# Kernel optimization log

Measured on AMD Instinct MI355X. Metric: run time of the kernel, lower is better.

Reference implementation:

```python
import jax, jax.numpy as jnp
import numpy as np

B, K, D, L = 512, 64, 1024, 8
LR, WD, STEPS = 1e-4, 0.01, 20


def setup_inputs() -> dict:
    key = jax.random.key(0)
    k1, k2, k3, k4, k5 = jax.random.split(key, 5)
    demo_embeddings = jax.random.normal(k1, (B, K, D), dtype=jnp.float32)
    demo_labels = jax.random.randint(k2, (B, K), 0, L, dtype=jnp.int32)
    embeddings = jax.random.normal(k3, (B, D), dtype=jnp.float32)
    # per-sample fresh nn.Linear init: U(-1/sqrt(D), 1/sqrt(D))
    bound = 1.0 / np.sqrt(D)
    W0 = jax.random.uniform(k4, (B, L, D), dtype=jnp.float32, minval=-bound, maxval=bound)
    b0 = jax.random.uniform(k5, (B, L), dtype=jnp.float32, minval=-bound, maxval=bound)
    return {"demo_embeddings": demo_embeddings, "embeddings": embeddings,
            "W0": W0, "b0": b0, "demo_labels": demo_labels}


def reference(demo_embeddings, embeddings, W0, b0, demo_labels):
    # one-hot targets for MSE branch: [B, K, L]
    Y = jax.nn.one_hot(demo_labels, L, dtype=jnp.float32)
    scale = 2.0 / (K * L)  # d(mean((out-Y)^2))/d(out) factor

    def sgd_step(carry, _):
        W, b = carry  # W: [B, L, D], b: [B, L]
        out = jnp.einsum('bkd,bld->bkl', demo_embeddings, W) + b[:, None, :]
        diff = out - Y
        gW = scale * jnp.einsum('bkl,bkd->bld', diff, demo_embeddings) + WD * W
        gb = scale * diff.sum(axis=1) + WD * b
        return (W - LR * gW, b - LR * gb), None

    (W, b), _ = jax.lax.scan(sgd_step, (W0, b0), None, length=STEPS)
    # predict each query with its own trained linear model
    logits = jnp.einsum('bd,bld->bl', embeddings, W) + b  # [B, L]
    return logits
```

## Files before the change

kernel.cpp:

```cpp
#include <hip/hip_runtime.h>


#define BB 512
#define KK 64
#define DD 1024
#define LL 8
#define NSTEPS 20

typedef __attribute__((ext_vector_type(8))) short bf16x8;
typedef __attribute__((ext_vector_type(4))) float f32x4;

__device__ __forceinline__ short f2bf(float f) {
    unsigned u = __float_as_uint(f);
    unsigned r = (u + 0x7FFFu + ((u >> 16) & 1u)) >> 16;
    return (short)r;
}

struct Chunk {
    float4 x0, x1, x2, x3;
    float4 p;
};

__global__ __launch_bounds__(256, 2)
void knn_linear_fix_kernel(const float* __restrict__ demo,
                           const float* __restrict__ emb,
                           const float* __restrict__ W0,
                           const float* __restrict__ b0,
                           const int*   __restrict__ labels,
                           float* __restrict__ out)
{
    const int b    = blockIdx.x;
    const int t    = threadIdx.x;
    const int lane = t & 63;
    const int wid  = t >> 6;
    const int lg   = lane >> 4;
    const int lr   = lane & 15;

    const float LR  = 1e-4f;
    const float WD  = 0.01f;
    const float LRS = LR * (2.0f / (float)(KK * LL));
    const float CD  = 1.0f - LR * WD;

    __shared__ short Xs[64 * 72];
    __shared__ short Ps[16 * 72];
    __shared__ short Gs[64 * 72];
    __shared__ short Ss[16 * 72];
    __shared__ float red[256];
    __shared__ float p0_s[16];
    __shared__ float q_s[64];
    __shared__ int   lab_s[64];

    const float* Xg = demo + (size_t)b * (KK * DD);
    const float* Wg = W0   + (size_t)b * (LL * DD);
    const float* eg = emb  + (size_t)b * DD;

    if (t < 64) lab_s[t] = labels[b * KK + t];
    for (int i = t; i < 16 * 72; i += 256) Ss[i] = 0;

    float bc = (lr < 8) ? b0[b * LL + lr] : 0.0f;

    f32x4 accG0 = {0,0,0,0}, accG1 = {0,0,0,0}, accG2 = {0,0,0,0}, accG3 = {0,0,0,0};
    f32x4 accM  = {0,0,0,0}, accPP = {0,0,0,0};

    const int xr = t >> 4;
    const int xc = (t & 15) * 4;

#define LOADX(buf, CH) do {                                                      \
        const int dk = (CH) * 64;                                                \
        (buf).x0 = *(const float4*)(Xg + (size_t)(xr     ) * DD + dk + xc);      \
        (buf).x1 = *(const float4*)(Xg + (size_t)(xr + 16) * DD + dk + xc);      \
        (buf).x2 = *(const float4*)(Xg + (size_t)(xr + 32) * DD + dk + xc);      \
        (buf).x3 = *(const float4*)(Xg + (size_t)(xr + 48) * DD + dk + xc);      \
        if (xr < 8)       (buf).p = *(const float4*)(Wg + (size_t)xr * DD + dk + xc); \
        else if (xr == 8) (buf).p = *(const float4*)(eg + dk + xc);              \
        else              (buf).p = make_float4(0.f, 0.f, 0.f, 0.f);             \
    } while (0)

#define STOREC(buf) do {                                                         \
        short4 h;                                                                \
        h.x = f2bf((buf).x0.x); h.y = f2bf((buf).x0.y);                          \
        h.z = f2bf((buf).x0.z); h.w = f2bf((buf).x0.w);                          \
        *(short4*)(&Xs[(xr     ) * 72 + xc]) = h;                                \
        h.x = f2bf((buf).x1.x); h.y = f2bf((buf).x1.y);                          \
        h.z = f2bf((buf).x1.z); h.w = f2bf((buf).x1.w);                          \
        *(short4*)(&Xs[(xr + 16) * 72 + xc]) = h;                                \
        h.x = f2bf((buf).x2.x); h.y = f2bf((buf).x2.y);                          \
        h.z = f2bf((buf).x2.z); h.w = f2bf((buf).x2.w);                          \
        *(short4*)(&Xs[(xr + 32) * 72 + xc]) = h;                                \
        h.x = f2bf((buf).x3.x); h.y = f2bf((buf).x3.y);                          \
        h.z = f2bf((buf).x3.z); h.w = f2bf((buf).x3.w);                          \
        *(short4*)(&Xs[(xr + 48) * 72 + xc]) = h;                                \
        h.x = f2bf((buf).p.x);  h.y = f2bf((buf).p.y);                           \
        h.z = f2bf((buf).p.z);  h.w = f2bf((buf).p.w);                           \
        *(short4*)(&Ps[xr * 72 + xc]) = h;                                       \
    } while (0)

#define MFMA_BODY() do {                                                         \
        _Pragma("unroll")                                                        \
        for (int ks = 0; ks < 2; ++ks) {                                         \
            const int ko = ks * 32 + lg * 8;                                     \
            const bf16x8 fa = *(const bf16x8*)(&Xs[(wid * 16 + lr) * 72 + ko]);  \
            const bf16x8 f0 = *(const bf16x8*)(&Xs[( 0 + lr) * 72 + ko]);        \
            const bf16x8 f1 = *(const bf16x8*)(&Xs[(16 + lr) * 72 + ko]);        \
            const bf16x8 f2 = *(const bf16x8*)(&Xs[(32 + lr) * 72 + ko]);        \
            const bf16x8 f3 = *(const bf16x8*)(&Xs[(48 + lr) * 72 + ko]);        \
            const bf16x8 fp = *(const bf16x8*)(&Ps[lr * 72 + ko]);               \
            accG0 = __builtin_amdgcn_mfma_f32_16x16x32_bf16(fa, f0, accG0, 0, 0, 0); \
            accG1 = __builtin_amdgcn_mfma_f32_16x16x32_bf16(fa, f1, accG1, 0, 0, 0); \
            accG2 = __builtin_amdgcn_mfma_f32_16x16x32_bf16(fa, f2, accG2, 0, 0, 0); \
            accG3 = __builtin_amdgcn_mfma_f32_16x16x32_bf16(fa, f3, accG3, 0, 0, 0); \
            accM  = __builtin_amdgcn_mfma_f32_16x16x32_bf16(fa, fp, accM , 0, 0, 0); \
            accPP = __builtin_amdgcn_mfma_f32_16x16x32_bf16(fp, fp, accPP, 0, 0, 0); \
        }                                                                        \
    } while (0)

    Chunk c0, c1, c2, c3;
    LOADX(c0, 0); LOADX(c1, 1); LOADX(c2, 2); LOADX(c3, 3);
    for (int ch = 0; ch < 16; ch += 4) {
        STOREC(c0); __syncthreads();
        if (ch + 4 < 16) LOADX(c0, ch + 4);
        MFMA_BODY(); __syncthreads();

        STOREC(c1); __syncthreads();
        if (ch + 5 < 16) LOADX(c1, ch + 5);
        MFMA_BODY(); __syncthreads();

        STOREC(c2); __syncthreads();
        if (ch + 6 < 16) LOADX(c2, ch + 6);
        MFMA_BODY(); __syncthreads();

        STOREC(c3); __syncthreads();
        if (ch + 7 < 16) LOADX(c3, ch + 7);
        MFMA_BODY(); __syncthreads();
    }

    #pragma unroll
    for (int r = 0; r < 4; ++r) {
        const int row = wid * 16 + lg * 4 + r;
        Gs[row * 72 +  0 + lr] = f2bf(accG0[r]);
        Gs[row * 72 + 16 + lr] = f2bf(accG1[r]);
        Gs[row * 72 + 32 + lr] = f2bf(accG2[r]);
        Gs[row * 72 + 48 + lr] = f2bf(accG3[r]);
    }
    if (lr == 8) {
        #pragma unroll
        for (int r = 0; r < 4; ++r) q_s[wid * 16 + lg * 4 + r] = accM[r];
    }
    if (wid == 0 && lg == 2) p0_s[lr] = accPP[0];
    __syncthreads();

    const bf16x8 ga0 = *(const bf16x8*)(&Gs[(wid * 16 + lr) * 72 +  0 + lg * 8]);
    const bf16x8 ga1 = *(const bf16x8*)(&Gs[(wid * 16 + lr) * 72 + 32 + lg * 8]);

    const int row0 = wid * 16 + lg * 4;
    const float yv0 = (lab_s[row0 + 0] == lr) ? 1.0f : 0.0f;
    const float yv1 = (lab_s[row0 + 1] == lr) ? 1.0f : 0.0f;
    const float yv2 = (lab_s[row0 + 2] == lr) ? 1.0f : 0.0f;
    const float yv3 = (lab_s[row0 + 3] == lr) ? 1.0f : 0.0f;

    const float m00 = accM[0], m01 = accM[1], m02 = accM[2], m03 = accM[3];
    float s0 = 0.f, s1 = 0.f, s2 = 0.f, s3 = 0.f;
    float ct = 1.0f;

    for (int step = 0; step < NSTEPS; ++step) {
        const bf16x8 sb0 = *(const bf16x8*)(&Ss[lr * 72 +  0 + lg * 8]);
        const bf16x8 sb1 = *(const bf16x8*)(&Ss[lr * 72 + 32 + lg * 8]);
        f32x4 o = {0.f, 0.f, 0.f, 0.f};
        o = __builtin_amdgcn_mfma_f32_16x16x32_bf16(ga0, sb0, o, 0, 0, 0);
        o = __builtin_amdgcn_mfma_f32_16x16x32_bf16(ga1, sb1, o, 0, 0, 0);
        const float d0 = ct * m00 + o[0] + bc - yv0;
        const float d1 = ct * m01 + o[1] + bc - yv1;
        const float d2 = ct * m02 + o[2] + bc - yv2;
        const float d3 = ct * m03 + o[3] + bc - yv3;
        s0 = CD * s0 - LRS * d0;
        s1 = CD * s1 - LRS * d1;
        s2 = CD * s2 - LRS * d2;
        s3 = CD * s3 - LRS * d3;
        ct *= CD;
        float colp = d0 + d1 + d2 + d3;
        colp += __shfl_xor(colp, 16, 64);
        colp += __shfl_xor(colp, 32, 64);
        __syncthreads();
        short4 sp;
        sp.x = f2bf(s0); sp.y = f2bf(s1); sp.z = f2bf(s2); sp.w = f2bf(s3);
        *(short4*)(&Ss[lr * 72 + row0]) = sp;
        if (lg == 0) red[wid * 16 + lr] = colp;
        __syncthreads();
        bc = CD * bc - LRS * (red[0 * 16 + lr] + red[1 * 16 + lr] +
                              red[2 * 16 + lr] + red[3 * 16 + lr]);
    }

    const float part = q_s[row0 + 0] * s0 + q_s[row0 + 1] * s1 +
                       q_s[row0 + 2] * s2 + q_s[row0 + 3] * s3;
    __syncthreads();
    red[(wid * 4 + lg) * 16 + lr] = part;
    __syncthreads();
    if (t < 8) {
        float a = 0.f;
        #pragma unroll
        for (int i = 0; i < 16; ++i) a += red[i * 16 + t];
        out[b * LL + t] = ct * p0_s[t] + a + bc;
    }
}

extern "C" void kernel_launch(void* const* d_in, const int* in_sizes, int n_in,
                              void* d_out, int out_size, void* d_ws, size_t ws_size,
                              hipStream_t stream) {
    const float* demo   = (const float*)d_in[0];
    const float* emb    = (const float*)d_in[1];
    const float* W0     = (const float*)d_in[2];
    const float* b0     = (const float*)d_in[3];
    const int*   labels = (const int*)d_in[4];
    float* out = (float*)d_out;
    (void)in_sizes; (void)n_in; (void)out_size; (void)d_ws; (void)ws_size;
    hipLaunchKernelGGL(knn_linear_fix_kernel, dim3(BB), dim3(256), 0, stream,
                       demo, emb, W0, b0, labels, out);
}
```

Measured before the change: 35.56 us.

## Double block to 512 threads and split Gram tile columns across wave pairs

Launches 512 threads per block (8 waves) instead of 256 and splits each wave's Gram-matrix work into a row tile plus a column-pair half, so each wave issues fewer MFMAs per chunk. The K-chunk width grows from 64 to 128 (8 chunks instead of 16), halving the number of barrier-separated store/compute phases, and the M projections move through shared memory so all waves can read them. The goal is more waves to hide global-load latency during the bandwidth-bound X streaming phase. In exchange, the 20-step SGD loop now has half its waves idle yet still paying every barrier, and each thread keeps a larger register and shared-memory footprint, which may limit how many blocks fit per CU.

```diff
diff --git a/kernel.cpp b/kernel.cpp
--- a/kernel.cpp
+++ b/kernel.cpp
@@ -6,6 +6,9 @@
 #define DD 1024
 #define LL 8
 #define NSTEPS 20
+#define BKC 128
+#define NCH (DD / BKC)
+#define XST 136
 
 typedef __attribute__((ext_vector_type(8))) short bf16x8;
 typedef __attribute__((ext_vector_type(4))) float f32x4;
@@ -21,7 +24,7 @@
     float4 p;
 };
 
-__global__ __launch_bounds__(256, 2)
+__global__ __launch_bounds__(512, 4)
 void knn_linear_fix_kernel(const float* __restrict__ demo,
                            const float* __restrict__ emb,
                            const float* __restrict__ W0,
@@ -35,38 +38,32 @@
     const int wid  = t >> 6;
     const int lg   = lane >> 4;
     const int lr   = lane & 15;
+    const int rt   = wid & 3;
+    const int cp   = wid >> 2;
 
     const float LR  = 1e-4f;
     const float WD  = 0.01f;
     const float LRS = LR * (2.0f / (float)(KK * LL));
     const float CD  = 1.0f - LR * WD;
 
-    __shared__ short Xs[64 * 72];
-    __shared__ short Ps[16 * 72];
+    __shared__ short Xs[64 * XST];
+    __shared__ short Ps[16 * XST];
     __shared__ short Gs[64 * 72];
     __shared__ short Ss[16 * 72];
+    __shared__ float Ms[64 * 16];
     __shared__ float red[256];
     __shared__ float p0_s[16];
-    __shared__ float q_s[64];
     __shared__ int   lab_s[64];
 
     const float* Xg = demo + (size_t)b * (KK * DD);
     const float* Wg = W0   + (size_t)b * (LL * DD);
     const float* eg = emb  + (size_t)b * DD;
 
-    if (t < 64) lab_s[t] = labels[b * KK + t];
-    for (int i = t; i < 16 * 72; i += 256) Ss[i] = 0;
-
-    float bc = (lr < 8) ? b0[b * LL + lr] : 0.0f;
-
-    f32x4 accG0 = {0,0,0,0}, accG1 = {0,0,0,0}, accG2 = {0,0,0,0}, accG3 = {0,0,0,0};
-    f32x4 accM  = {0,0,0,0}, accPP = {0,0,0,0};
-
-    const int xr = t >> 4;
-    const int xc = (t & 15) * 4;
+    const int xr = t >> 5;
+    const int xc = (t & 31) * 4;
 
 #define LOADX(buf, CH) do {                                                      \
-        const int dk = (CH) * 64;                                                \
+        const int dk = (CH) * BKC;                                               \
         (buf).x0 = *(const float4*)(Xg + (size_t)(xr     ) * DD + dk + xc);      \
         (buf).x1 = *(const float4*)(Xg + (size_t)(xr + 16) * DD + dk + xc);      \
         (buf).x2 = *(const float4*)(Xg + (size_t)(xr + 32) * DD + dk + xc);      \
@@ -80,85 +77,95 @@
         short4 h;                                                                \
         h.x = f2bf((buf).x0.x); h.y = f2bf((buf).x0.y);                          \
         h.z = f2bf((buf).x0.z); h.w = f2bf((buf).x0.w);                          \
-        *(short4*)(&Xs[(xr     ) * 72 + xc]) = h;                                \
+        *(short4*)(&Xs[(xr     ) * XST + xc]) = h;                               \
         h.x = f2bf((buf).x1.x); h.y = f2bf((buf).x1.y);                          \
         h.z = f2bf((buf).x1.z); h.w = f2bf((buf).x1.w);                          \
-        *(short4*)(&Xs[(xr + 16) * 72 + xc]) = h;                                \
+        *(short4*)(&Xs[(xr + 16) * XST + xc]) = h;                               \
         h.x = f2bf((buf).x2.x); h.y = f2bf((buf).x2.y);                          \
         h.z = f2bf((buf).x2.z); h.w = f2bf((buf).x2.w);                          \
-        *(short4*)(&Xs[(xr + 32) * 72 + xc]) = h;                                \
+        *(short4*)(&Xs[(xr + 32) * XST + xc]) = h;                               \
         h.x = f2bf((buf).x3.x); h.y = f2bf((buf).x3.y);                          \
         h.z = f2bf((buf).x3.z); h.w = f2bf((buf).x3.w);                          \
-        *(short4*)(&Xs[(xr + 48) * 72 + xc]) = h;                                \
+        *(short4*)(&Xs[(xr + 48) * XST + xc]) = h;                               \
         h.x = f2bf((buf).p.x);  h.y = f2bf((buf).p.y);                           \
         h.z = f2bf((buf).p.z);  h.w = f2bf((buf).p.w);                           \
-        *(short4*)(&Ps[xr * 72 + xc]) = h;                                       \
+        *(short4*)(&Ps[xr * XST + xc]) = h;                                      \
     } while (0)
 
 #define MFMA_BODY() do {                                                         \
         _Pragma("unroll")                                                        \
-        for (int ks = 0; ks < 2; ++ks) {                                         \
+        for (int ks = 0; ks < 4; ++ks) {                                         \
             const int ko = ks * 32 + lg * 8;                                     \
-            const bf16x8 fa = *(const bf16x8*)(&Xs[(wid * 16 + lr) * 72 + ko]);  \
-            const bf16x8 f0 = *(const bf16x8*)(&Xs[( 0 + lr) * 72 + ko]);        \
-            const bf16x8 f1 = *(const bf16x8*)(&Xs[(16 + lr) * 72 + ko]);        \
-            const bf16x8 f2 = *(const bf16x8*)(&Xs[(32 + lr) * 72 + ko]);        \
-            const bf16x8 f3 = *(const bf16x8*)(&Xs[(48 + lr) * 72 + ko]);        \
-            const bf16x8 fp = *(const bf16x8*)(&Ps[lr * 72 + ko]);               \
-            accG0 = __builtin_amdgcn_mfma_f32_16x16x32_bf16(fa, f0, accG0, 0, 0, 0); \
-            accG1 = __builtin_amdgcn_mfma_f32_16x16x32_bf16(fa, f1, accG1, 0, 0, 0); \
-            accG2 = __builtin_amdgcn_mfma_f32_16x16x32_bf16(fa, f2, accG2, 0, 0, 0); \
-            accG3 = __builtin_amdgcn_mfma_f32_16x16x32_bf16(fa, f3, accG3, 0, 0, 0); \
-            accM  = __builtin_amdgcn_mfma_f32_16x16x32_bf16(fa, fp, accM , 0, 0, 0); \
-            accPP = __builtin_amdgcn_mfma_f32_16x16x32_bf16(fp, fp, accPP, 0, 0, 0); \
+            const bf16x8 fa  = *(const bf16x8*)(&Xs[(rt * 16 + lr) * XST + ko]); \
+            const bf16x8 fb0 = *(const bf16x8*)(&Xs[((cp * 2    ) * 16 + lr) * XST + ko]); \
+            const bf16x8 fb1 = *(const bf16x8*)(&Xs[((cp * 2 + 1) * 16 + lr) * XST + ko]); \
+            accG0 = __builtin_amdgcn_mfma_f32_16x16x32_bf16(fa, fb0, accG0, 0, 0, 0); \
+            accG1 = __builtin_amdgcn_mfma_f32_16x16x32_bf16(fa, fb1, accG1, 0, 0, 0); \
+            if (cp == 0) {                                                       \
+                const bf16x8 fp = *(const bf16x8*)(&Ps[lr * XST + ko]);          \
+                accM = __builtin_amdgcn_mfma_f32_16x16x32_bf16(fa, fp, accM, 0, 0, 0); \
+                if (wid == 0)                                                    \
+                    accPP = __builtin_amdgcn_mfma_f32_16x16x32_bf16(fp, fp, accPP, 0, 0, 0); \
+            }                                                                    \
         }                                                                        \
     } while (0)
 
     Chunk c0, c1, c2, c3;
     LOADX(c0, 0); LOADX(c1, 1); LOADX(c2, 2); LOADX(c3, 3);
-    for (int ch = 0; ch < 16; ch += 4) {
+
+    if (t < 64) lab_s[t] = labels[b * KK + t];
+    for (int i = t; i < 16 * 72; i += 512) Ss[i] = 0;
+    float bc = (lr < 8) ? b0[b * LL + lr] : 0.0f;
+
+    f32x4 accG0 = {0,0,0,0}, accG1 = {0,0,0,0};
+    f32x4 accM  = {0,0,0,0}, accPP = {0,0,0,0};
+
+    for (int ch = 0; ch < NCH; ch += 4) {
         STOREC(c0); __syncthreads();
-        if (ch + 4 < 16) LOADX(c0, ch + 4);
+        if (ch + 4 < NCH) LOADX(c0, ch + 4);
         MFMA_BODY(); __syncthreads();
 
         STOREC(c1); __syncthreads();
-        if (ch + 5 < 16) LOADX(c1, ch + 5);
+        if (ch + 5 < NCH) LOADX(c1, ch + 5);
         MFMA_BODY(); __syncthreads();
 
         STOREC(c2); __syncthreads();
-        if (ch + 6 < 16) LOADX(c2, ch + 6);
+        if (ch + 6 < NCH) LOADX(c2, ch + 6);
         MFMA_BODY(); __syncthreads();
 
         STOREC(c3); __syncthreads();
-        if (ch + 7 < 16) LOADX(c3, ch + 7);
+        if (ch + 7 < NCH) LOADX(c3, ch + 7);
         MFMA_BODY(); __syncthreads();
     }
 
     #pragma unroll
     for (int r = 0; r < 4; ++r) {
-        const int row = wid * 16 + lg * 4 + r;
-        Gs[row * 72 +  0 + lr] = f2bf(accG0[r]);
-        Gs[row * 72 + 16 + lr] = f2bf(accG1[r]);
-        Gs[row * 72 + 32 + lr] = f2bf(accG2[r]);
-        Gs[row * 72 + 48 + lr] = f2bf(accG3[r]);
-    }
-    if (lr == 8) {
+        const int row = rt * 16 + lg * 4 + r;
+        Gs[row * 72 + (cp * 2    ) * 16 + lr] = f2bf(accG0[r]);
+        Gs[row * 72 + (cp * 2 + 1) * 16 + lr] = f2bf(accG1[r]);
+    }
+    if (cp == 0) {
         #pragma unroll
-        for (int r = 0; r < 4; ++r) q_s[wid * 16 + lg * 4 + r] = accM[r];
+        for (int r = 0; r < 4; ++r)
+            Ms[(rt * 16 + lg * 4 + r) * 16 + lr] = accM[r];
     }
     if (wid == 0 && lg == 2) p0_s[lr] = accPP[0];
     __syncthreads();
 
-    const bf16x8 ga0 = *(const bf16x8*)(&Gs[(wid * 16 + lr) * 72 +  0 + lg * 8]);
-    const bf16x8 ga1 = *(const bf16x8*)(&Gs[(wid * 16 + lr) * 72 + 32 + lg * 8]);
-
-    const int row0 = wid * 16 + lg * 4;
+    const bf16x8 ga0 = *(const bf16x8*)(&Gs[(rt * 16 + lr) * 72 +  0 + lg * 8]);
+    const bf16x8 ga1 = *(const bf16x8*)(&Gs[(rt * 16 + lr) * 72 + 32 + lg * 8]);
+
+    const int row0 = rt * 16 + lg * 4;
     const float yv0 = (lab_s[row0 + 0] == lr) ? 1.0f : 0.0f;
     const float yv1 = (lab_s[row0 + 1] == lr) ? 1.0f : 0.0f;
     const float yv2 = (lab_s[row0 + 2] == lr) ? 1.0f : 0.0f;
     const float yv3 = (lab_s[row0 + 3] == lr) ? 1.0f : 0.0f;
 
-    const float m00 = accM[0], m01 = accM[1], m02 = accM[2], m03 = accM[3];
+    const float m00 = Ms[(row0 + 0) * 16 + lr];
+    const float m01 = Ms[(row0 + 1) * 16 + lr];
+    const float m02 = Ms[(row0 + 2) * 16 + lr];
+    const float m03 = Ms[(row0 + 3) * 16 + lr];
+
     float s0 = 0.f, s1 = 0.f, s2 = 0.f, s3 = 0.f;
     float ct = 1.0f;
 
@@ -181,19 +188,21 @@
         colp += __shfl_xor(colp, 16, 64);
         colp += __shfl_xor(colp, 32, 64);
         __syncthreads();
-        short4 sp;
-        sp.x = f2bf(s0); sp.y = f2bf(s1); sp.z = f2bf(s2); sp.w = f2bf(s3);
-        *(short4*)(&Ss[lr * 72 + row0]) = sp;
-        if (lg == 0) red[wid * 16 + lr] = colp;
+        if (wid < 4) {
+            short4 sp;
+            sp.x = f2bf(s0); sp.y = f2bf(s1); sp.z = f2bf(s2); sp.w = f2bf(s3);
+            *(short4*)(&Ss[lr * 72 + row0]) = sp;
+            if (lg == 0) red[wid * 16 + lr] = colp;
+        }
         __syncthreads();
         bc = CD * bc - LRS * (red[0 * 16 + lr] + red[1 * 16 + lr] +
                               red[2 * 16 + lr] + red[3 * 16 + lr]);
     }
 
-    const float part = q_s[row0 + 0] * s0 + q_s[row0 + 1] * s1 +
-                       q_s[row0 + 2] * s2 + q_s[row0 + 3] * s3;
+    const float part = Ms[(row0 + 0) * 16 + 8] * s0 + Ms[(row0 + 1) * 16 + 8] * s1 +
+                       Ms[(row0 + 2) * 16 + 8] * s2 + Ms[(row0 + 3) * 16 + 8] * s3;
     __syncthreads();
-    red[(wid * 4 + lg) * 16 + lr] = part;
+    if (wid < 4) red[(wid * 4 + lg) * 16 + lr] = part;
     __syncthreads();
     if (t < 8) {
         float a = 0.f;
@@ -213,6 +222,6 @@
     const int*   labels = (const int*)d_in[4];
     float* out = (float*)d_out;
     (void)in_sizes; (void)n_in; (void)out_size; (void)d_ws; (void)ws_size;
-    hipLaunchKernelGGL(knn_linear_fix_kernel, dim3(BB), dim3(256), 0, stream,
+    hipLaunchKernelGGL(knn_linear_fix_kernel, dim3(BB), dim3(512), 0, stream,
                        demo, emb, W0, b0, labels, out);
 }
```

Result: slower. 41.33 us (+16.2%).

## Double-buffer LDS staging and halve barriers in the Gram accumulation loop

Applied to the files above, without the earlier changes.

Uses two LDS buffers for the bf16 X/P chunks, so the next chunk is converted and stored while MFMAs read the current one. This removes one of the two block barriers per chunk. Barriers become raw s_barrier calls with an explicit lgkmcnt wait and sched_barrier fences. The label, bias and Ss initialisation moves after the first global loads so it overlaps their latency. It costs extra LDS, which may affect two-blocks-per-CU occupancy, and the sched barriers constrain compiler scheduling.

```diff
diff --git a/kernel.cpp b/kernel.cpp
--- a/kernel.cpp
+++ b/kernel.cpp
@@ -20,6 +20,13 @@
     float4 x0, x1, x2, x3;
     float4 p;
 };
+
+#define PIPE_SYNC() do {                                      \
+        __builtin_amdgcn_sched_barrier(0);                    \
+        asm volatile("s_waitcnt lgkmcnt(0)" ::: "memory");    \
+        __builtin_amdgcn_s_barrier();                         \
+        __builtin_amdgcn_sched_barrier(0);                    \
+    } while (0)
 
 __global__ __launch_bounds__(256, 2)
 void knn_linear_fix_kernel(const float* __restrict__ demo,
@@ -41,8 +48,8 @@
     const float LRS = LR * (2.0f / (float)(KK * LL));
     const float CD  = 1.0f - LR * WD;
 
-    __shared__ short Xs[64 * 72];
-    __shared__ short Ps[16 * 72];
+    __shared__ short Xs[2][64 * 72];
+    __shared__ short Ps[2][16 * 72];
     __shared__ short Gs[64 * 72];
     __shared__ short Ss[16 * 72];
     __shared__ float red[256];
@@ -53,14 +60,6 @@
     const float* Xg = demo + (size_t)b * (KK * DD);
     const float* Wg = W0   + (size_t)b * (LL * DD);
     const float* eg = emb  + (size_t)b * DD;
-
-    if (t < 64) lab_s[t] = labels[b * KK + t];
-    for (int i = t; i < 16 * 72; i += 256) Ss[i] = 0;
-
-    float bc = (lr < 8) ? b0[b * LL + lr] : 0.0f;
-
-    f32x4 accG0 = {0,0,0,0}, accG1 = {0,0,0,0}, accG2 = {0,0,0,0}, accG3 = {0,0,0,0};
-    f32x4 accM  = {0,0,0,0}, accPP = {0,0,0,0};
 
     const int xr = t >> 4;
     const int xc = (t & 15) * 4;
@@ -76,35 +75,35 @@
         else              (buf).p = make_float4(0.f, 0.f, 0.f, 0.f);             \
     } while (0)
 
-#define STOREC(buf) do {                                                         \
+#define STOREC(buf, BI) do {                                                     \
         short4 h;                                                                \
         h.x = f2bf((buf).x0.x); h.y = f2bf((buf).x0.y);                          \
         h.z = f2bf((buf).x0.z); h.w = f2bf((buf).x0.w);                          \
-        *(short4*)(&Xs[(xr     ) * 72 + xc]) = h;                                \
+        *(short4*)(&Xs[BI][(xr     ) * 72 + xc]) = h;                            \
         h.x = f2bf((buf).x1.x); h.y = f2bf((buf).x1.y);                          \
         h.z = f2bf((buf).x1.z); h.w = f2bf((buf).x1.w);                          \
-        *(short4*)(&Xs[(xr + 16) * 72 + xc]) = h;                                \
+        *(short4*)(&Xs[BI][(xr + 16) * 72 + xc]) = h;                            \
         h.x = f2bf((buf).x2.x); h.y = f2bf((buf).x2.y);                          \
         h.z = f2bf((buf).x2.z); h.w = f2bf((buf).x2.w);                          \
-        *(short4*)(&Xs[(xr + 32) * 72 + xc]) = h;                                \
+        *(short4*)(&Xs[BI][(xr + 32) * 72 + xc]) = h;                            \
         h.x = f2bf((buf).x3.x); h.y = f2bf((buf).x3.y);                          \
         h.z = f2bf((buf).x3.z); h.w = f2bf((buf).x3.w);                          \
-        *(short4*)(&Xs[(xr + 48) * 72 + xc]) = h;                                \
+        *(short4*)(&Xs[BI][(xr + 48) * 72 + xc]) = h;                            \
         h.x = f2bf((buf).p.x);  h.y = f2bf((buf).p.y);                           \
         h.z = f2bf((buf).p.z);  h.w = f2bf((buf).p.w);                           \
-        *(short4*)(&Ps[xr * 72 + xc]) = h;                                       \
-    } while (0)
-
-#define MFMA_BODY() do {                                                         \
+        *(short4*)(&Ps[BI][xr * 72 + xc]) = h;                                   \
+    } while (0)
+
+#define MFMA_BODY(BI) do {                                                       \
         _Pragma("unroll")                                                        \
         for (int ks = 0; ks < 2; ++ks) {                                         \
             const int ko = ks * 32 + lg * 8;                                     \
-            const bf16x8 fa = *(const bf16x8*)(&Xs[(wid * 16 + lr) * 72 + ko]);  \
-            const bf16x8 f0 = *(const bf16x8*)(&Xs[( 0 + lr) * 72 + ko]);        \
-            const bf16x8 f1 = *(const bf16x8*)(&Xs[(16 + lr) * 72 + ko]);        \
-            const bf16x8 f2 = *(const bf16x8*)(&Xs[(32 + lr) * 72 + ko]);        \
-            const bf16x8 f3 = *(const bf16x8*)(&Xs[(48 + lr) * 72 + ko]);        \
-            const bf16x8 fp = *(const bf16x8*)(&Ps[lr * 72 + ko]);               \
+            const bf16x8 fa = *(const bf16x8*)(&Xs[BI][(wid * 16 + lr) * 72 + ko]); \
+            const bf16x8 f0 = *(const bf16x8*)(&Xs[BI][( 0 + lr) * 72 + ko]);    \
+            const bf16x8 f1 = *(const bf16x8*)(&Xs[BI][(16 + lr) * 72 + ko]);    \
+            const bf16x8 f2 = *(const bf16x8*)(&Xs[BI][(32 + lr) * 72 + ko]);    \
+            const bf16x8 f3 = *(const bf16x8*)(&Xs[BI][(48 + lr) * 72 + ko]);    \
+            const bf16x8 fp = *(const bf16x8*)(&Ps[BI][lr * 72 + ko]);           \
             accG0 = __builtin_amdgcn_mfma_f32_16x16x32_bf16(fa, f0, accG0, 0, 0, 0); \
             accG1 = __builtin_amdgcn_mfma_f32_16x16x32_bf16(fa, f1, accG1, 0, 0, 0); \
             accG2 = __builtin_amdgcn_mfma_f32_16x16x32_bf16(fa, f2, accG2, 0, 0, 0); \
@@ -116,22 +115,36 @@
 
     Chunk c0, c1, c2, c3;
     LOADX(c0, 0); LOADX(c1, 1); LOADX(c2, 2); LOADX(c3, 3);
+
+    if (t < 64) lab_s[t] = labels[b * KK + t];
+    for (int i = t; i < 16 * 72; i += 256) Ss[i] = 0;
+    float bc = (lr < 8) ? b0[b * LL + lr] : 0.0f;
+
+    f32x4 accG0 = {0,0,0,0}, accG1 = {0,0,0,0}, accG2 = {0,0,0,0}, accG3 = {0,0,0,0};
+    f32x4 accM  = {0,0,0,0}, accPP = {0,0,0,0};
+
+    STOREC(c0, 0);
+    PIPE_SYNC();
+    LOADX(c0, 4);
+
     for (int ch = 0; ch < 16; ch += 4) {
-        STOREC(c0); __syncthreads();
-        if (ch + 4 < 16) LOADX(c0, ch + 4);
-        MFMA_BODY(); __syncthreads();
-
-        STOREC(c1); __syncthreads();
-        if (ch + 5 < 16) LOADX(c1, ch + 5);
-        MFMA_BODY(); __syncthreads();
-
-        STOREC(c2); __syncthreads();
-        if (ch + 6 < 16) LOADX(c2, ch + 6);
-        MFMA_BODY(); __syncthreads();
-
-        STOREC(c3); __syncthreads();
-        if (ch + 7 < 16) LOADX(c3, ch + 7);
-        MFMA_BODY(); __syncthreads();
+        MFMA_BODY(0);
+        STOREC(c1, 1); if (ch + 5 < 16) LOADX(c1, ch + 5);
+        PIPE_SYNC();
+
+        MFMA_BODY(1);
+        STOREC(c2, 0); if (ch + 6 < 16) LOADX(c2, ch + 6);
+        PIPE_SYNC();
+
+        MFMA_BODY(0);
+        STOREC(c3, 1); if (ch + 7 < 16) LOADX(c3, ch + 7);
+        PIPE_SYNC();
+
+        MFMA_BODY(1);
+        if (ch + 4 < 16) {
+            STOREC(c0, 0); if (ch + 8 < 16) LOADX(c0, ch + 8);
+        }
+        PIPE_SYNC();
     }
 
     #pragma unroll
```

New measurement: 35.63 us. About the same (+0.2%).
